# Kernel optimization log

Hardware: AMD Instinct MI355X
Metric: run time of the kernel (lower is better)

## Reference

```python
import jax, jax.numpy as jnp
import numpy as np

B_SZ, C_IN, C_OUT, H, W = 16, 32, 32, 128, 128
K, CODE, PAD, FACTOR = 3, 2, 1, 1.0

def setup_inputs() -> dict:
    key = jax.random.key(0)
    ks = jax.random.split(key, 7)
    s = 0.05
    return {
        "x": jax.random.normal(ks[0], (B_SZ, C_IN, H, W), jnp.float32),
        "codes": jax.random.normal(ks[1], (B_SZ, CODE, CODE), jnp.float32),
        "weight": jax.random.normal(ks[2], (C_OUT, C_IN, K, K), jnp.float32) * s,
        "A": jax.random.normal(ks[3], (C_IN, CODE, K, K), jnp.float32) * s,
        "Bm": jax.random.normal(ks[4], (C_OUT, CODE, K, K), jnp.float32) * s,
        "bias": jax.random.normal(ks[5], (C_OUT,), jnp.float32) * s,
        "bias_context": jax.random.normal(ks[6], (CODE, C_OUT), jnp.float32) * s,
    }

def reference(x, codes, weight, A, Bm, bias, bias_context):
    # hypernetwork weight synthesis: [b, out, in, k, k]
    w_ctx = jnp.einsum('ickl,bcr->birkl', A, codes)            # [b, in, code, k, k]
    w_ctx = jnp.einsum('birkl,orkl->boikl', w_ctx, Bm)         # [b, out, in, k, k]
    combined_weight = weight[None] + FACTOR * w_ctx
    # per-sample bias from diagonal of codes
    diag = jnp.diagonal(codes, axis1=-2, axis2=-1)             # [b, code]
    combined_bias = bias[None] + FACTOR * (diag @ bias_context)  # [b, out]
    # circular padding then per-sample VALID conv (== unfold + einsum)
    xp = jnp.pad(x, ((0, 0), (0, 0), (PAD, PAD), (PAD, PAD)), mode='wrap')
    def conv_one(xi, wi):
        return jax.lax.conv_general_dilated(
            xi[None], wi, window_strides=(1, 1), padding='VALID',
            dimension_numbers=('NCHW', 'OIHW', 'NCHW'))[0]
    out = jax.vmap(conv_one)(xp, combined_weight)              # [b, out, H, W]
    return out + combined_bias[:, :, None, None]
```

## Files before the change

kernel.cpp:

```cpp
#include <hip/hip_runtime.h>

typedef short bf16x8 __attribute__((ext_vector_type(8)));
typedef float f32x4  __attribute__((ext_vector_type(4)));
typedef unsigned int u32;

#define HH 128
#define WW 128

__device__ __forceinline__ u32 cvt_pk_bf16(float lo, float hi) {
    u32 r;
    asm volatile("v_cvt_pk_bf16_f32 %0, %1, %2" : "=v"(r) : "v"(lo), "v"(hi));
    return r;
}

__device__ __forceinline__ void lds_barrier() {
    asm volatile("s_waitcnt lgkmcnt(0)" ::: "memory");
    __builtin_amdgcn_s_barrier();
    __builtin_amdgcn_sched_barrier(0);
}

__global__ __launch_bounds__(1024, 1) void geps_mfma_kernel(
    const float* __restrict__ x, const float* __restrict__ codes,
    const float* __restrict__ weight, const float* __restrict__ A,
    const float* __restrict__ Bm, const float* __restrict__ bias,
    const float* __restrict__ bctx, float* __restrict__ out)
{
    __shared__ bf16x8 lds_x[5120];
    __shared__ bf16x8 lds_w[1152];
    __shared__ float  lds_ctx[576];
    __shared__ float  lds_b[32];

    const int tid  = threadIdx.x;
    const int l    = tid & 63;
    const int wvid = tid >> 6;
    const int row  = wvid >> 1;
    const int nh   = wvid & 1;

    const int orig = blockIdx.x;
    const int vb   = (orig & 7) * 32 + (orig >> 3);
    const int b    = vb >> 4;
    const int grp  = vb & 15;
    const int h0   = grp * 8;

    float2 f[5][4];
    #pragma unroll
    for (int it = 0; it < 5; ++it) {
        int idx = it * 1024 + tid;
        int cp = idx & 63, jh = (idx >> 6) & 1, ig = (idx >> 7) & 3, rr = idx >> 9;
        int grow = (h0 - 1 + rr) & 127;
        const float* src =
            x + ((size_t)(b * 32 + ig * 8 + jh * 4) * HH + grow) * WW + cp * 2;
        #pragma unroll
        for (int jj = 0; jj < 4; ++jj)
            f[it][jj] = *(const float2*)(src + (size_t)jj * HH * WW);
    }

    const float c00 = codes[b * 4 + 0];
    const float c01 = codes[b * 4 + 1];
    const float c10 = codes[b * 4 + 2];
    const float c11 = codes[b * 4 + 3];
    if (tid < 576) {
        int j = tid;
        int i = j / 18, rem = j % 18, r = rem / 9, kl = rem % 9;
        float a0 = A[(i * 2 + 0) * 9 + kl];
        float a1 = A[(i * 2 + 1) * 9 + kl];
        lds_ctx[j] = (r == 0) ? (a0 * c00 + a1 * c10) : (a0 * c01 + a1 * c11);
    }
    if (tid < 32) lds_b[tid] = bias[tid] + c00 * bctx[tid] + c11 * bctx[32 + tid];
    lds_barrier();

    for (int j = tid; j < 1152; j += 1024) {
        int kl = j >> 7, rem = j & 127, o = rem >> 2, kb = rem & 3;
        float m0 = Bm[(o * 2 + 0) * 9 + kl];
        float m1 = Bm[(o * 2 + 1) * 9 + kl];
        float wf[8];
        #pragma unroll
        for (int jj = 0; jj < 8; ++jj) {
            int i = kb * 8 + jj;
            wf[jj] = weight[(o * 32 + i) * 9 + kl]
                   + lds_ctx[i * 18 + kl] * m0
                   + lds_ctx[i * 18 + 9 + kl] * m1;
        }
        u32 pk[4];
        #pragma unroll
        for (int q = 0; q < 4; ++q) pk[q] = cvt_pk_bf16(wf[2 * q], wf[2 * q + 1]);
        *(uint4*)&lds_w[kl * 128 + (o >> 4) * 64 + kb * 16 + (o & 15)] =
            make_uint4(pk[0], pk[1], pk[2], pk[3]);
    }

    #pragma unroll
    for (int it = 0; it < 5; ++it) {
        int idx = it * 1024 + tid;
        int cp = idx & 63, jh = (idx >> 6) & 1, ig = (idx >> 7) & 3, rr = idx >> 9;
        int c0 = cp * 2;
        u32 a0 = cvt_pk_bf16(f[it][0].x, f[it][1].x);
        u32 a1 = cvt_pk_bf16(f[it][2].x, f[it][3].x);
        u32 b0 = cvt_pk_bf16(f[it][0].y, f[it][1].y);
        u32 b1 = cvt_pk_bf16(f[it][2].y, f[it][3].y);
        int didx = (c0 >> 4) * 64 + ig * 16 + (c0 & 15);
        *(uint2*)((char*)lds_x + rr * 8192 + didx * 16 + jh * 8) =
            make_uint2(a0, a1);
        *(uint2*)((char*)lds_x + rr * 8192 + (didx + 1) * 16 + jh * 8) =
            make_uint2(b0, b1);
    }
    lds_barrier();

    const int awb = (l >> 4) * 16 + (l & 15);
    bf16x8 af[9][2];
    #pragma unroll
    for (int kl = 0; kl < 9; ++kl)
        #pragma unroll
        for (int oh = 0; oh < 2; ++oh)
            af[kl][oh] = lds_w[kl * 128 + oh * 64 + awb];

    const int p = l & 15, igf = l >> 4;
    int bb[3];
    #pragma unroll
    for (int dl = -1; dl <= 1; ++dl) {
        int pq = p + dl;
        bb[dl + 1] = (pq & 15) + ((pq >> 4) << 6) + igf * 16;
    }

    float blr[2][4];
    #pragma unroll
    for (int oh = 0; oh < 2; ++oh)
        #pragma unroll
        for (int r = 0; r < 4; ++r)
            blr[oh][r] = lds_b[oh * 16 + (l >> 4) * 4 + r];

    f32x4 acc[2][4];
    #pragma unroll
    for (int oh = 0; oh < 2; ++oh)
        #pragma unroll
        for (int q = 0; q < 4; ++q) acc[oh][q] = (f32x4){0.f, 0.f, 0.f, 0.f};

    #pragma unroll
    for (int lc = 0; lc < 3; ++lc) {
        #pragma unroll
        for (int k = 0; k < 3; ++k) {
            const bf16x8 a0 = af[k * 3 + lc][0];
            const bf16x8 a1 = af[k * 3 + lc][1];
            #pragma unroll
            for (int q = 0; q < 4; ++q) {
                int t = (bb[lc] + (nh * 4 + q) * 64) & 511;
                bf16x8 bfv = lds_x[(row + k) * 512 + t];
                acc[0][q] = __builtin_amdgcn_mfma_f32_16x16x32_bf16(
                    a0, bfv, acc[0][q], 0, 0, 0);
                acc[1][q] = __builtin_amdgcn_mfma_f32_16x16x32_bf16(
                    a1, bfv, acc[1][q], 0, 0, 0);
            }
        }
    }

    float* bounce = (float*)lds_x;
    #pragma unroll
    for (int oh = 0; oh < 2; ++oh) {
        lds_barrier();
        #pragma unroll
        for (int q = 0; q < 4; ++q)
            #pragma unroll
            for (int r = 0; r < 4; ++r) {
                int o16  = (l >> 4) * 4 + r;
                int col  = (nh * 4 + q) * 16 + (l & 15);
                int col2 = (col + o16 * 4) & 127;
                bounce[(o16 * 8 + row) * 128 + col2] = acc[oh][q][r] + blr[oh][r];
            }
        lds_barrier();
        const int ch = oh * 16 + wvid;
        #pragma unroll
        for (int k = 0; k < 4; ++k) {
            int hrow = 2 * k + (l >> 5);
            int lcol = (l & 31) * 4;
            int pcol = (lcol + wvid * 4) & 127;
            f32x4 v = *(const f32x4*)&bounce[(wvid * 8 + hrow) * 128 + pcol];
            __builtin_nontemporal_store(
                v, (f32x4*)&out[((size_t)(b * 32 + ch) * HH + (h0 + hrow)) * WW +
                                lcol]);
        }
    }
}

extern "C" void kernel_launch(void* const* d_in, const int* in_sizes, int n_in,
                              void* d_out, int out_size, void* d_ws, size_t ws_size,
                              hipStream_t stream) {
    const float* x      = (const float*)d_in[0];
    const float* codes  = (const float*)d_in[1];
    const float* weight = (const float*)d_in[2];
    const float* A      = (const float*)d_in[3];
    const float* Bm     = (const float*)d_in[4];
    const float* bias   = (const float*)d_in[5];
    const float* bctx   = (const float*)d_in[6];
    float* out = (float*)d_out;

    hipLaunchKernelGGL(geps_mfma_kernel, dim3(256), dim3(1024), 0, stream,
                       x, codes, weight, A, Bm, bias, bctx, out);
}
```

Measured before the change: 21.40 us.

## Halve block tile to four rows, launch 512 blocks of 512 threads

Each block now covers 4 output rows instead of 8, so the launch grows to 512 blocks of 512 threads with launch bounds allowing two blocks per CU, and LDS for the input tile shrinks accordingly. The second half of the weight fragments is now read from LDS inside the MFMA loop instead of being held in registers, which lowers register pressure. The aim is more resident waves and better overlap across blocks. The cost is a larger halo overhead (6 loaded rows per 4 output rows instead of 10 per 8), weight synthesis repeated by twice as many blocks, and extra LDS reads in the inner loop.

Measured after the change: 23.88 us. 11.6% more time.

```diff
diff --git a/kernel.cpp b/kernel.cpp
--- a/kernel.cpp
+++ b/kernel.cpp
@@ -19,13 +19,13 @@
     __builtin_amdgcn_sched_barrier(0);
 }
 
-__global__ __launch_bounds__(1024, 1) void geps_mfma_kernel(
+__global__ __launch_bounds__(512, 2) void geps_mfma_kernel(
     const float* __restrict__ x, const float* __restrict__ codes,
     const float* __restrict__ weight, const float* __restrict__ A,
     const float* __restrict__ Bm, const float* __restrict__ bias,
     const float* __restrict__ bctx, float* __restrict__ out)
 {
-    __shared__ bf16x8 lds_x[5120];
+    __shared__ bf16x8 lds_x[3072];
     __shared__ bf16x8 lds_w[1152];
     __shared__ float  lds_ctx[576];
     __shared__ float  lds_b[32];
@@ -33,19 +33,19 @@
     const int tid  = threadIdx.x;
     const int l    = tid & 63;
     const int wvid = tid >> 6;
-    const int row  = wvid >> 1;
+    const int row4 = wvid >> 1;
     const int nh   = wvid & 1;
 
     const int orig = blockIdx.x;
-    const int vb   = (orig & 7) * 32 + (orig >> 3);
-    const int b    = vb >> 4;
-    const int grp  = vb & 15;
-    const int h0   = grp * 8;
+    const int vb   = (orig & 7) * 64 + (orig >> 3);
+    const int b    = vb >> 5;
+    const int grp  = vb & 31;
+    const int h0   = grp * 4;
 
-    float2 f[5][4];
+    float2 f[6][4];
     #pragma unroll
-    for (int it = 0; it < 5; ++it) {
-        int idx = it * 1024 + tid;
+    for (int it = 0; it < 6; ++it) {
+        int idx = it * 512 + tid;
         int cp = idx & 63, jh = (idx >> 6) & 1, ig = (idx >> 7) & 3, rr = idx >> 9;
         int grow = (h0 - 1 + rr) & 127;
         const float* src =
@@ -59,8 +59,7 @@
     const float c01 = codes[b * 4 + 1];
     const float c10 = codes[b * 4 + 2];
     const float c11 = codes[b * 4 + 3];
-    if (tid < 576) {
-        int j = tid;
+    for (int j = tid; j < 576; j += 512) {
         int i = j / 18, rem = j % 18, r = rem / 9, kl = rem % 9;
         float a0 = A[(i * 2 + 0) * 9 + kl];
         float a1 = A[(i * 2 + 1) * 9 + kl];
@@ -69,7 +68,7 @@
     if (tid < 32) lds_b[tid] = bias[tid] + c00 * bctx[tid] + c11 * bctx[32 + tid];
     lds_barrier();
 
-    for (int j = tid; j < 1152; j += 1024) {
+    for (int j = tid; j < 1152; j += 512) {
         int kl = j >> 7, rem = j & 127, o = rem >> 2, kb = rem & 3;
         float m0 = Bm[(o * 2 + 0) * 9 + kl];
         float m1 = Bm[(o * 2 + 1) * 9 + kl];
@@ -89,8 +88,8 @@
     }
 
     #pragma unroll
-    for (int it = 0; it < 5; ++it) {
-        int idx = it * 1024 + tid;
+    for (int it = 0; it < 6; ++it) {
+        int idx = it * 512 + tid;
         int cp = idx & 63, jh = (idx >> 6) & 1, ig = (idx >> 7) & 3, rr = idx >> 9;
         int c0 = cp * 2;
         u32 a0 = cvt_pk_bf16(f[it][0].x, f[it][1].x);
@@ -106,12 +105,10 @@
     lds_barrier();
 
     const int awb = (l >> 4) * 16 + (l & 15);
-    bf16x8 af[9][2];
+    bf16x8 af0[9];
     #pragma unroll
     for (int kl = 0; kl < 9; ++kl)
-        #pragma unroll
-        for (int oh = 0; oh < 2; ++oh)
-            af[kl][oh] = lds_w[kl * 128 + oh * 64 + awb];
+        af0[kl] = lds_w[kl * 128 + awb];
 
     const int p = l & 15, igf = l >> 4;
     int bb[3];
@@ -138,12 +135,13 @@
     for (int lc = 0; lc < 3; ++lc) {
         #pragma unroll
         for (int k = 0; k < 3; ++k) {
-            const bf16x8 a0 = af[k * 3 + lc][0];
-            const bf16x8 a1 = af[k * 3 + lc][1];
+            const bf16x8 a0 = af0[k * 3 + lc];
+            const bf16x8 a1 = lds_w[(k * 3 + lc) * 128 + 64 + awb];
+            const int s = row4 + k;
             #pragma unroll
             for (int q = 0; q < 4; ++q) {
                 int t = (bb[lc] + (nh * 4 + q) * 64) & 511;
-                bf16x8 bfv = lds_x[(row + k) * 512 + t];
+                bf16x8 bfv = lds_x[s * 512 + t];
                 acc[0][q] = __builtin_amdgcn_mfma_f32_16x16x32_bf16(
                     a0, bfv, acc[0][q], 0, 0, 0);
                 acc[1][q] = __builtin_amdgcn_mfma_f32_16x16x32_bf16(
@@ -163,19 +161,23 @@
                 int o16  = (l >> 4) * 4 + r;
                 int col  = (nh * 4 + q) * 16 + (l & 15);
                 int col2 = (col + o16 * 4) & 127;
-                bounce[(o16 * 8 + row) * 128 + col2] = acc[oh][q][r] + blr[oh][r];
+                bounce[(o16 * 4 + row4) * 128 + col2] = acc[oh][q][r] + blr[oh][r];
             }
         lds_barrier();
-        const int ch = oh * 16 + wvid;
         #pragma unroll
-        for (int k = 0; k < 4; ++k) {
-            int hrow = 2 * k + (l >> 5);
-            int lcol = (l & 31) * 4;
-            int pcol = (lcol + wvid * 4) & 127;
-            f32x4 v = *(const f32x4*)&bounce[(wvid * 8 + hrow) * 128 + pcol];
-            __builtin_nontemporal_store(
-                v, (f32x4*)&out[((size_t)(b * 32 + ch) * HH + (h0 + hrow)) * WW +
-                                lcol]);
+        for (int c2 = 0; c2 < 2; ++c2) {
+            const int o16 = wvid * 2 + c2;
+            const int ch  = oh * 16 + o16;
+            #pragma unroll
+            for (int k2 = 0; k2 < 2; ++k2) {
+                int hrow = 2 * k2 + (l >> 5);
+                int lcol = (l & 31) * 4;
+                int pcol = (lcol + o16 * 4) & 127;
+                f32x4 v = *(const f32x4*)&bounce[(o16 * 4 + hrow) * 128 + pcol];
+                __builtin_nontemporal_store(
+                    v, (f32x4*)&out[((size_t)(b * 32 + ch) * HH + (h0 + hrow)) *
+                                    WW + lcol]);
+            }
         }
     }
 }
@@ -192,6 +194,6 @@
     const float* bctx   = (const float*)d_in[6];
     float* out = (float*)d_out;
 
-    hipLaunchKernelGGL(geps_mfma_kernel, dim3(256), dim3(1024), 0, stream,
+    hipLaunchKernelGGL(geps_mfma_kernel, dim3(512), dim3(512), 0, stream,
                        x, codes, weight, A, Bm, bias, bctx, out);
 }
```
